# Performance work log

Measured on AMD Instinct MI355X. Metric: run time of the kernel, lower is better.

Reference implementation:

```python
import jax, jax.numpy as jnp
import numpy as np

B, N, F, H, N_ITERS = 32, 256, 8, 256, 3


def setup_inputs() -> dict:
    key = jax.random.key(0)
    ks = jax.random.split(key, 10)
    sc = lambda k, shape, fan: (jax.random.normal(k, shape, jnp.float32) / np.sqrt(fan).astype(np.float32))
    return {
        "jets": jax.random.normal(ks[0], (B, N, F), jnp.float32),
        "W_emb": sc(ks[1], (F, H), F), "b_emb": jnp.zeros((H,), jnp.float32),
        "w_edge": sc(ks[2], (H,), H), "b_edge": jnp.zeros((), jnp.float32),
        "W_msg": sc(ks[3], (H, H), H), "b_msg": jnp.zeros((H,), jnp.float32),
        "Wi": sc(ks[4], (3 * H, H + F), H + F), "bi": jnp.zeros((3 * H,), jnp.float32),
        "Wh": sc(ks[5], (3 * H, H), H), "bh": jnp.zeros((3 * H,), jnp.float32),
        "Wr1": sc(ks[6], (H, H), H), "br1": jnp.zeros((H,), jnp.float32),
        "Wr2": sc(ks[7], (H, H), H), "br2": jnp.zeros((H,), jnp.float32),
    }


def _gru(x, h, Wi, bi, Wh, bh):
    # standard torch GRUCell math; x: [B,N,H+F], h: [B,N,H]
    gi = x @ Wi.T + bi
    gh = h @ Wh.T + bh
    ir, iz, inew = jnp.split(gi, 3, axis=-1)
    hr, hz, hnew = jnp.split(gh, 3, axis=-1)
    r = jax.nn.sigmoid(ir + hr)
    z = jax.nn.sigmoid(iz + hz)
    n = jnp.tanh(inew + r * hnew)
    return (1.0 - z) * n + z * h


def reference(jets, W_emb, b_emb, w_edge, b_edge, W_msg, b_msg, Wi, bi, Wh, bh, Wr1, br1, Wr2, br2):
    h = jnp.tanh(jets @ W_emb + b_emb)  # [B,N,H]
    for _ in range(N_ITERS):
        # edge_embedding(h_l + h_r) is affine -> (h_i + h_j).w + b = s_i + s_j + b,
        # avoiding the [B,N,N,H] broadcast intermediate while computing identical scores.
        s = h @ w_edge  # [B,N]
        scores = s[:, :, None] + s[:, None, :] + b_edge  # [B,N,N]
        A = jax.nn.softmax(scores, axis=2)  # attention over sender nodes j
        msg = jnp.tanh(jnp.einsum('bij,bjh->bih', A, h @ W_msg + b_msg))
        h = _gru(jnp.concatenate([msg, jets], axis=-1), h, Wi, bi, Wh, bh)
    x = jax.nn.relu(h @ Wr1 + br1) @ Wr2 + br2  # DTNN readout per node
    return jnp.sum(x, axis=1)  # [B,H] summed over vertices
```

## Files before the change

kernel.cpp:

```cpp
#include <hip/hip_runtime.h>
#include <math.h>

#define NT 256

typedef __attribute__((ext_vector_type(8))) short short8;
typedef __attribute__((ext_vector_type(4))) float f32x4;
typedef unsigned short ushort_t;

__device__ __forceinline__ float sigmoidf_(float x){ return 1.0f/(1.0f+__expf(-x)); }
__device__ __forceinline__ ushort_t f2bf(float x){
  unsigned int u = __float_as_uint(x);
  u = u + 0x7fff + ((u>>16)&1);
  return (ushort_t)(u>>16);
}
__device__ __forceinline__ float bf2f(ushort_t b){
  return __uint_as_float(((unsigned int)b)<<16);
}

__global__ __launch_bounds__(256) void k_pe(
    const float* __restrict__ jets, const float* __restrict__ W_emb,
    const float* __restrict__ b_emb, const float* __restrict__ w_edge,
    const float* __restrict__ Wi, const float* __restrict__ bi,
    const float* __restrict__ Wh, const float* __restrict__ Wr1,
    ushort_t* __restrict__ hbf0, ushort_t* __restrict__ gjets,
    float* __restrict__ WiMt, ushort_t* __restrict__ WhB,
    ushort_t* __restrict__ Wr1T, float* __restrict__ s_part)
{
  int t = threadIdx.x, blk = blockIdx.x;
  int gid = blk*NT + t, gstride = gridDim.x*NT;
  for (int e=gid; e<256*768; e+=gstride){ int k=e/768, row=e-k*768; WiMt[e]=Wi[(size_t)row*264 + k]; }
  for (int e=gid; e<768*256; e+=gstride){ WhB[e]=f2bf(Wh[e]); }
  for (int e=gid; e<256*256; e+=gstride){ int n=e>>8, k=e&255; Wr1T[e]=f2bf(Wr1[(size_t)k*256+n]); }
  int lane = t & 63, w = t >> 6;
  #pragma unroll
  for (int v=0; v<4; ++v){
    int m = blk*16 + w*4 + v;
    float jr[8];
    #pragma unroll
    for (int f=0; f<8; ++f) jr[f] = jets[m*8+f];
    float sp = 0.f;
    #pragma unroll
    for (int u=0; u<4; ++u){
      int c = lane + 64*u;
      float a = b_emb[c];
      #pragma unroll
      for (int f=0; f<8; ++f) a = fmaf(jr[f], W_emb[f*256+c], a);
      float hv = tanhf(a);
      hbf0[(size_t)m*256 + c] = f2bf(hv);
      sp = fmaf(hv, w_edge[c], sp);
    }
    sp += __shfl_xor(sp,1); sp += __shfl_xor(sp,2); sp += __shfl_xor(sp,4);
    sp += __shfl_xor(sp,8); sp += __shfl_xor(sp,16); sp += __shfl_xor(sp,32);
    if (lane==0) s_part[m] = sp;
    else if (lane<8) s_part[lane*8192 + m] = 0.f;
    #pragma unroll
    for (int g=0; g<3; ++g){
      #pragma unroll
      for (int u=0; u<4; ++u){
        int c = lane + 64*u;
        int rowi = g*256 + c;
        float acc = bi[rowi];
        #pragma unroll
        for (int f=0; f<8; ++f) acc = fmaf(jr[f], Wi[(size_t)rowi*264 + 256 + f], acc);
        gjets[(size_t)m*768 + rowi] = f2bf(acc);
      }
    }
  }
}

__global__ __launch_bounds__(256) void k_hbar(const ushort_t* __restrict__ hbf,
    const float* __restrict__ s_part, float* __restrict__ hbar_p){
  int t = threadIdx.x;
  int b = blockIdx.x >> 3, js = blockIdx.x & 7;
  int jc = js << 5;
  __shared__ float eS[256], red[256];
  float s_t = 0.f;
  #pragma unroll
  for (int sl=0; sl<8; ++sl) s_t += s_part[sl*8192 + b*256 + t];
  red[t] = s_t; __syncthreads();
  for (int o=128;o>0;o>>=1){ if (t<o) red[t]=fmaxf(red[t],red[t+o]); __syncthreads(); }
  float mx = red[0]; __syncthreads();
  float e = __expf(s_t-mx); eS[t]=e; red[t]=e; __syncthreads();
  for (int o=128;o>0;o>>=1){ if (t<o) red[t]+=red[t+o]; __syncthreads(); }
  float rZ = 1.0f/red[0];
  const ushort_t* hb = hbf + (size_t)b*256*256;
  float p = 0.f;
  #pragma unroll
  for (int j=0;j<32;++j)
    p = fmaf(eS[jc+j], bf2f(hb[(size_t)(jc+j)*256 + t]), p);
  hbar_p[js*8192 + b*256 + t] = p*rZ;
}

__global__ __launch_bounds__(256) void k_msgp(const float* __restrict__ hbar_p,
    const float* __restrict__ W_msg, float* __restrict__ msg_p){
  int t = threadIdx.x;
  int b = blockIdx.x >> 3, ks = blockIdx.x & 7;
  __shared__ float hch[32];
  if (t < 32){
    float v = 0.f;
    #pragma unroll
    for (int sl=0; sl<8; ++sl) v += hbar_p[sl*8192 + b*256 + ks*32 + t];
    hch[t] = v;
  }
  __syncthreads();
  float acc = 0.f;
  #pragma unroll
  for (int k=0; k<32; ++k)
    acc = fmaf(hch[k], W_msg[(size_t)(ks*32+k)*256 + t], acc);
  msg_p[ks*8192 + b*256 + t] = acc;
}

__global__ __launch_bounds__(256) void k_gmsgp(const float* __restrict__ msg_p,
    const float* __restrict__ b_msg, const float* __restrict__ WiMt,
    float* __restrict__ gmsg_p){
  int t = threadIdx.x;
  int b = blockIdx.x >> 3, ks = blockIdx.x & 7;
  __shared__ float mch[32];
  if (t < 32){
    float v = b_msg[ks*32 + t];
    #pragma unroll
    for (int sl=0; sl<8; ++sl) v += msg_p[sl*8192 + b*256 + ks*32 + t];
    mch[t] = tanhf(v);
  }
  __syncthreads();
  float a0=0.f, a1=0.f, a2=0.f;
  #pragma unroll
  for (int k=0; k<32; ++k){
    float m = mch[k];
    const float* wr = &WiMt[(size_t)(ks*32+k)*768 + t];
    a0 = fmaf(m, wr[0],   a0);
    a1 = fmaf(m, wr[256], a1);
    a2 = fmaf(m, wr[512], a2);
  }
  float* gp = &gmsg_p[(size_t)ks*24576 + (size_t)b*768 + t];
  gp[0] = a0; gp[256] = a1; gp[512] = a2;
}

__global__ __launch_bounds__(256) void k_gru_mfma(
    const ushort_t* __restrict__ hbf_in,
    const ushort_t* __restrict__ WhB, const float* __restrict__ bh,
    const ushort_t* __restrict__ gjets, const float* __restrict__ gmsg_p,
    const float* __restrict__ w_edge,
    ushort_t* __restrict__ hbf_out, float* __restrict__ s_part, int compute_s)
{
  __shared__ __align__(16) short As[64*32];
  __shared__ __align__(16) short Bs[3*64*32];
  __shared__ float gm_s[192], bh_s[192];
  int t = threadIdx.x;
  int hcb = blockIdx.x & 3, mblk = blockIdx.x >> 2;
  int m0 = mblk*64, hc0 = hcb*64, b = m0 >> 8;
  if (t < 192){
    int g = t>>6, c = t&63;
    int rowi = g*256 + hc0 + c;
    float acc = 0.f;
    #pragma unroll
    for (int sl=0; sl<8; ++sl) acc += gmsg_p[(size_t)sl*24576 + (size_t)b*768 + rowi];
    gm_s[t] = acc;
    bh_s[t] = bh[rowi];
  }
  int lane = t & 63, w = t >> 6;
  int wr = w >> 1, wc = w & 1;
  int q = lane >> 4, r = lane & 15;
  int srow = t >> 2, sseg = t & 3;
  f32x4 acc[3][2][2] = {};
  for (int kt = 0; kt < 8; ++kt){
    __syncthreads();
    *(uint4*)&As[t*8] = *(const uint4*)&hbf_in[(size_t)(m0+srow)*256 + kt*32 + sseg*8];
    #pragma unroll
    for (int g = 0; g < 3; ++g)
      *(uint4*)&Bs[g*2048 + t*8] = *(const uint4*)&WhB[(size_t)(g*256 + hc0 + srow)*256 + kt*32 + sseg*8];
    __syncthreads();
    short8 af[2], bfr[3][2];
    #pragma unroll
    for (int fm=0; fm<2; ++fm)
      af[fm] = *(const short8*)&As[(wr*32 + fm*16 + r)*32 + q*8];
    #pragma unroll
    for (int g=0; g<3; ++g)
      #pragma unroll
      for (int fn=0; fn<2; ++fn)
        bfr[g][fn] = *(const short8*)&Bs[g*2048 + (wc*32 + fn*16 + r)*32 + q*8];
    #pragma unroll
    for (int g=0; g<3; ++g)
      #pragma unroll
      for (int fm=0; fm<2; ++fm)
        #pragma unroll
        for (int fn=0; fn<2; ++fn)
          acc[g][fm][fn] = __builtin_amdgcn_mfma_f32_16x16x32_bf16(af[fm], bfr[g][fn], acc[g][fm][fn], 0,0,0);
  }
  float wef[2];
  wef[0] = w_edge[hc0 + wc*32 + r];
  wef[1] = w_edge[hc0 + wc*32 + 16 + r];
  float pacc[2][4] = {};
  #pragma unroll
  for (int fm=0; fm<2; ++fm)
    #pragma unroll
    for (int fn=0; fn<2; ++fn){
      int cloc = wc*32 + fn*16 + r;
      int hcol = hc0 + cloc;
      #pragma unroll
      for (int jj=0; jj<4; ++jj){
        int m = m0 + wr*32 + fm*16 + q*4 + jj;
        float gir = bf2f(gjets[(size_t)m*768 + hcol])       + gm_s[cloc];
        float giz = bf2f(gjets[(size_t)m*768 + 256 + hcol]) + gm_s[64+cloc];
        float gin = bf2f(gjets[(size_t)m*768 + 512 + hcol]) + gm_s[128+cloc];
        float rr = sigmoidf_(gir + acc[0][fm][fn][jj] + bh_s[cloc]);
        float zz = sigmoidf_(giz + acc[1][fm][fn][jj] + bh_s[64+cloc]);
        float nn = tanhf(gin + rr*(acc[2][fm][fn][jj] + bh_s[128+cloc]));
        float ho = bf2f(hbf_in[(size_t)m*256 + hcol]);
        float hn = (1.f - zz)*nn + zz*ho;
        hbf_out[(size_t)m*256 + hcol] = f2bf(hn);
        pacc[fm][jj] = fmaf(wef[fn], hn, pacc[fm][jj]);
      }
    }
  if (compute_s){
    #pragma unroll
    for (int fm=0; fm<2; ++fm)
      #pragma unroll
      for (int jj=0; jj<4; ++jj){
        float p = pacc[fm][jj];
        p += __shfl_xor(p,1); p += __shfl_xor(p,2);
        p += __shfl_xor(p,4); p += __shfl_xor(p,8);
        if (r == 0)
          s_part[(hcb*2 + wc)*8192 + m0 + wr*32 + fm*16 + q*4 + jj] = p;
      }
  }
}

__global__ __launch_bounds__(256) void k_ro(
    const ushort_t* __restrict__ hbf, const ushort_t* __restrict__ Wr1T,
    const float* __restrict__ br1, float* __restrict__ zsum_p)
{
  __shared__ __align__(16) short As[64*32];
  __shared__ __align__(16) short Bs[64*32];
  int t = threadIdx.x;
  int ncb = blockIdx.x & 3, mblk = blockIdx.x >> 2;
  int m0 = mblk*64, nc0 = ncb*64, b = m0 >> 8;
  int lane = t & 63, w = t >> 6;
  int wr = w >> 1, wc = w & 1;
  int q = lane >> 4, r = lane & 15;
  int srow = t >> 2, sseg = t & 3;
  f32x4 acc[2][2] = {};
  for (int kt = 0; kt < 8; ++kt){
    __syncthreads();
    *(uint4*)&As[t*8] = *(const uint4*)&hbf[(size_t)(m0+srow)*256 + kt*32 + sseg*8];
    *(uint4*)&Bs[t*8] = *(const uint4*)&Wr1T[(size_t)(nc0+srow)*256 + kt*32 + sseg*8];
    __syncthreads();
    short8 af[2], bfr[2];
    #pragma unroll
    for (int fm=0; fm<2; ++fm)
      af[fm] = *(const short8*)&As[(wr*32 + fm*16 + r)*32 + q*8];
    #pragma unroll
    for (int fn=0; fn<2; ++fn)
      bfr[fn] = *(const short8*)&Bs[(wc*32 + fn*16 + r)*32 + q*8];
    #pragma unroll
    for (int fm=0; fm<2; ++fm)
      #pragma unroll
      for (int fn=0; fn<2; ++fn)
        acc[fm][fn] = __builtin_amdgcn_mfma_f32_16x16x32_bf16(af[fm], bfr[fn], acc[fm][fn], 0,0,0);
  }
  #pragma unroll
  for (int fn=0; fn<2; ++fn){
    int n = nc0 + wc*32 + fn*16 + r;
    float bb = br1[n];
    float cs = 0.f;
    #pragma unroll
    for (int fm=0; fm<2; ++fm)
      #pragma unroll
      for (int jj=0; jj<4; ++jj)
        cs += fmaxf(acc[fm][fn][jj] + bb, 0.f);
    cs += __shfl_xor(cs, 16);
    cs += __shfl_xor(cs, 32);
    if (q == 0) zsum_p[((mblk&3)*2 + wr)*8192 + b*256 + n] = cs;
  }
}

__global__ __launch_bounds__(256) void k_fin(const float* __restrict__ zsum_p,
    const float* __restrict__ Wr2, const float* __restrict__ br2,
    float* __restrict__ out){
  int b = blockIdx.x, t = threadIdx.x;
  __shared__ float zs[256];
  float z = 0.f;
  #pragma unroll
  for (int sl=0; sl<8; ++sl) z += zsum_p[sl*8192 + b*256 + t];
  zs[t] = z; __syncthreads();
  float acc = 0.f;
  for (int k=0;k<256;++k) acc = fmaf(zs[k], Wr2[k*256 + t], acc);
  out[b*256 + t] = acc + 256.0f*br2[t];
}

extern "C" void kernel_launch(void* const* d_in, const int* in_sizes, int n_in,
                              void* d_out, int out_size, void* d_ws, size_t ws_size,
                              hipStream_t stream){
  (void)in_sizes; (void)n_in; (void)out_size; (void)ws_size;
  const float* jets  = (const float*)d_in[0];
  const float* W_emb = (const float*)d_in[1];
  const float* b_emb = (const float*)d_in[2];
  const float* w_edge= (const float*)d_in[3];
  const float* W_msg = (const float*)d_in[5];
  const float* b_msg = (const float*)d_in[6];
  const float* Wi    = (const float*)d_in[7];
  const float* bi    = (const float*)d_in[8];
  const float* Wh    = (const float*)d_in[9];
  const float* bh    = (const float*)d_in[10];
  const float* Wr1   = (const float*)d_in[11];
  const float* br1   = (const float*)d_in[12];
  const float* Wr2   = (const float*)d_in[13];
  const float* br2   = (const float*)d_in[14];
  float* out = (float*)d_out;
  float* ws  = (float*)d_ws;
  ushort_t* hbf0  = (ushort_t*)ws;
  ushort_t* hbf1  = (ushort_t*)(ws + 1048576);
  ushort_t* gjets = (ushort_t*)(ws + 2097152);
  float* WiMt     = ws + 5242880;
  ushort_t* WhB   = (ushort_t*)(ws + 5439488);
  ushort_t* Wr1T  = (ushort_t*)(ws + 5537792);
  float* s_part   = ws + 5570560;
  float* hbar_p   = ws + 5636096;
  float* msg_p    = ws + 5701632;
  float* gmsg_p   = ws + 5767168;
  float* zsum_p   = ws + 5963776;
  ushort_t* hbf[2] = {hbf0, hbf1};

  k_pe<<<512,NT,0,stream>>>(jets, W_emb, b_emb, w_edge, Wi, bi, Wh, Wr1,
                            hbf[0], gjets, WiMt, WhB, Wr1T, s_part);
  for (int it=0; it<3; ++it){
    int cur = it & 1, nxt = cur ^ 1;
    k_hbar<<<256,NT,0,stream>>>(hbf[cur], s_part, hbar_p);
    k_msgp<<<256,NT,0,stream>>>(hbar_p, W_msg, msg_p);
    k_gmsgp<<<256,NT,0,stream>>>(msg_p, b_msg, WiMt, gmsg_p);
    k_gru_mfma<<<512,NT,0,stream>>>(hbf[cur], WhB, bh, gjets, gmsg_p, w_edge,
                                    hbf[nxt], s_part, (it<2)?1:0);
  }
  k_ro<<<512,NT,0,stream>>>(hbf[1], Wr1T, br1, zsum_p);
  k_fin<<<32,NT,0,stream>>>(zsum_p, Wr2, br2, out);
}
```

Baseline: 125.9 us.

## Fuse msg-to-gate projection into GRU kernel and load MFMA operands directly

Removes the separate k_gmsgp launch per iteration. Each GRU block now reduces msg partials, applies tanh, and computes its 192 gate-message values against a bf16 copy of Wi's message columns. The GRU and readout MFMA kernels drop LDS staging and barriers and read A/B fragments straight from global memory (L2-resident). This trades three launches for redundant per-block dot products (256 serial k per thread, on 192 threads) and for uncoalesced short8 global loads in place of shared tiles. It also lowers the Wi message weights to bf16 precision.

```diff
diff --git a/kernel.cpp b/kernel.cpp
--- a/kernel.cpp
+++ b/kernel.cpp
@@ -23,12 +23,12 @@
     const float* __restrict__ Wi, const float* __restrict__ bi,
     const float* __restrict__ Wh, const float* __restrict__ Wr1,
     ushort_t* __restrict__ hbf0, ushort_t* __restrict__ gjets,
-    float* __restrict__ WiMt, ushort_t* __restrict__ WhB,
+    ushort_t* __restrict__ WiMtB, ushort_t* __restrict__ WhB,
     ushort_t* __restrict__ Wr1T, float* __restrict__ s_part)
 {
   int t = threadIdx.x, blk = blockIdx.x;
   int gid = blk*NT + t, gstride = gridDim.x*NT;
-  for (int e=gid; e<256*768; e+=gstride){ int k=e/768, row=e-k*768; WiMt[e]=Wi[(size_t)row*264 + k]; }
+  for (int e=gid; e<256*768; e+=gstride){ int k=e/768, row=e-k*768; WiMtB[e]=f2bf(Wi[(size_t)row*264 + k]); }
   for (int e=gid; e<768*256; e+=gstride){ WhB[e]=f2bf(Wh[e]); }
   for (int e=gid; e<256*256; e+=gstride){ int n=e>>8, k=e&255; Wr1T[e]=f2bf(Wr1[(size_t)k*256+n]); }
   int lane = t & 63, w = t >> 6;
@@ -110,75 +110,51 @@
   msg_p[ks*8192 + b*256 + t] = acc;
 }
 
-__global__ __launch_bounds__(256) void k_gmsgp(const float* __restrict__ msg_p,
-    const float* __restrict__ b_msg, const float* __restrict__ WiMt,
-    float* __restrict__ gmsg_p){
-  int t = threadIdx.x;
-  int b = blockIdx.x >> 3, ks = blockIdx.x & 7;
-  __shared__ float mch[32];
-  if (t < 32){
-    float v = b_msg[ks*32 + t];
-    #pragma unroll
-    for (int sl=0; sl<8; ++sl) v += msg_p[sl*8192 + b*256 + ks*32 + t];
-    mch[t] = tanhf(v);
-  }
-  __syncthreads();
-  float a0=0.f, a1=0.f, a2=0.f;
-  #pragma unroll
-  for (int k=0; k<32; ++k){
-    float m = mch[k];
-    const float* wr = &WiMt[(size_t)(ks*32+k)*768 + t];
-    a0 = fmaf(m, wr[0],   a0);
-    a1 = fmaf(m, wr[256], a1);
-    a2 = fmaf(m, wr[512], a2);
-  }
-  float* gp = &gmsg_p[(size_t)ks*24576 + (size_t)b*768 + t];
-  gp[0] = a0; gp[256] = a1; gp[512] = a2;
-}
-
 __global__ __launch_bounds__(256) void k_gru_mfma(
     const ushort_t* __restrict__ hbf_in,
     const ushort_t* __restrict__ WhB, const float* __restrict__ bh,
-    const ushort_t* __restrict__ gjets, const float* __restrict__ gmsg_p,
+    const ushort_t* __restrict__ gjets, const float* __restrict__ msg_p,
+    const float* __restrict__ b_msg, const ushort_t* __restrict__ WiMtB,
     const float* __restrict__ w_edge,
     ushort_t* __restrict__ hbf_out, float* __restrict__ s_part, int compute_s)
 {
-  __shared__ __align__(16) short As[64*32];
-  __shared__ __align__(16) short Bs[3*64*32];
+  __shared__ float mvS[256];
   __shared__ float gm_s[192], bh_s[192];
   int t = threadIdx.x;
   int hcb = blockIdx.x & 3, mblk = blockIdx.x >> 2;
   int m0 = mblk*64, hc0 = hcb*64, b = m0 >> 8;
+  {
+    float v = b_msg[t];
+    #pragma unroll
+    for (int sl=0; sl<8; ++sl) v += msg_p[sl*8192 + b*256 + t];
+    mvS[t] = tanhf(v);
+  }
+  __syncthreads();
   if (t < 192){
     int g = t>>6, c = t&63;
     int rowi = g*256 + hc0 + c;
     float acc = 0.f;
-    #pragma unroll
-    for (int sl=0; sl<8; ++sl) acc += gmsg_p[(size_t)sl*24576 + (size_t)b*768 + rowi];
+    #pragma unroll 8
+    for (int k=0; k<256; ++k)
+      acc = fmaf(mvS[k], bf2f(WiMtB[(size_t)k*768 + rowi]), acc);
     gm_s[t] = acc;
     bh_s[t] = bh[rowi];
   }
   int lane = t & 63, w = t >> 6;
   int wr = w >> 1, wc = w & 1;
   int q = lane >> 4, r = lane & 15;
-  int srow = t >> 2, sseg = t & 3;
   f32x4 acc[3][2][2] = {};
+  #pragma unroll
   for (int kt = 0; kt < 8; ++kt){
-    __syncthreads();
-    *(uint4*)&As[t*8] = *(const uint4*)&hbf_in[(size_t)(m0+srow)*256 + kt*32 + sseg*8];
-    #pragma unroll
-    for (int g = 0; g < 3; ++g)
-      *(uint4*)&Bs[g*2048 + t*8] = *(const uint4*)&WhB[(size_t)(g*256 + hc0 + srow)*256 + kt*32 + sseg*8];
-    __syncthreads();
     short8 af[2], bfr[3][2];
     #pragma unroll
     for (int fm=0; fm<2; ++fm)
-      af[fm] = *(const short8*)&As[(wr*32 + fm*16 + r)*32 + q*8];
+      af[fm] = *(const short8*)&hbf_in[(size_t)(m0 + wr*32 + fm*16 + r)*256 + kt*32 + q*8];
     #pragma unroll
     for (int g=0; g<3; ++g)
       #pragma unroll
       for (int fn=0; fn<2; ++fn)
-        bfr[g][fn] = *(const short8*)&Bs[g*2048 + (wc*32 + fn*16 + r)*32 + q*8];
+        bfr[g][fn] = *(const short8*)&WhB[(size_t)(g*256 + hc0 + wc*32 + fn*16 + r)*256 + kt*32 + q*8];
     #pragma unroll
     for (int g=0; g<3; ++g)
       #pragma unroll
@@ -187,6 +163,7 @@
         for (int fn=0; fn<2; ++fn)
           acc[g][fm][fn] = __builtin_amdgcn_mfma_f32_16x16x32_bf16(af[fm], bfr[g][fn], acc[g][fm][fn], 0,0,0);
   }
+  __syncthreads();
   float wef[2];
   wef[0] = w_edge[hc0 + wc*32 + r];
   wef[1] = w_edge[hc0 + wc*32 + 16 + r];
@@ -230,28 +207,22 @@
     const ushort_t* __restrict__ hbf, const ushort_t* __restrict__ Wr1T,
     const float* __restrict__ br1, float* __restrict__ zsum_p)
 {
-  __shared__ __align__(16) short As[64*32];
-  __shared__ __align__(16) short Bs[64*32];
   int t = threadIdx.x;
   int ncb = blockIdx.x & 3, mblk = blockIdx.x >> 2;
   int m0 = mblk*64, nc0 = ncb*64, b = m0 >> 8;
   int lane = t & 63, w = t >> 6;
   int wr = w >> 1, wc = w & 1;
   int q = lane >> 4, r = lane & 15;
-  int srow = t >> 2, sseg = t & 3;
   f32x4 acc[2][2] = {};
+  #pragma unroll
   for (int kt = 0; kt < 8; ++kt){
-    __syncthreads();
-    *(uint4*)&As[t*8] = *(const uint4*)&hbf[(size_t)(m0+srow)*256 + kt*32 + sseg*8];
-    *(uint4*)&Bs[t*8] = *(const uint4*)&Wr1T[(size_t)(nc0+srow)*256 + kt*32 + sseg*8];
-    __syncthreads();
     short8 af[2], bfr[2];
     #pragma unroll
     for (int fm=0; fm<2; ++fm)
-      af[fm] = *(const short8*)&As[(wr*32 + fm*16 + r)*32 + q*8];
+      af[fm] = *(const short8*)&hbf[(size_t)(m0 + wr*32 + fm*16 + r)*256 + kt*32 + q*8];
     #pragma unroll
     for (int fn=0; fn<2; ++fn)
-      bfr[fn] = *(const short8*)&Bs[(wc*32 + fn*16 + r)*32 + q*8];
+      bfr[fn] = *(const short8*)&Wr1T[(size_t)(nc0 + wc*32 + fn*16 + r)*256 + kt*32 + q*8];
     #pragma unroll
     for (int fm=0; fm<2; ++fm)
       #pragma unroll
@@ -311,25 +282,23 @@
   ushort_t* hbf0  = (ushort_t*)ws;
   ushort_t* hbf1  = (ushort_t*)(ws + 1048576);
   ushort_t* gjets = (ushort_t*)(ws + 2097152);
-  float* WiMt     = ws + 5242880;
-  ushort_t* WhB   = (ushort_t*)(ws + 5439488);
-  ushort_t* Wr1T  = (ushort_t*)(ws + 5537792);
-  float* s_part   = ws + 5570560;
-  float* hbar_p   = ws + 5636096;
-  float* msg_p    = ws + 5701632;
-  float* gmsg_p   = ws + 5767168;
-  float* zsum_p   = ws + 5963776;
+  ushort_t* WiMtB = (ushort_t*)(ws + 5242880);
+  ushort_t* WhB   = (ushort_t*)(ws + 5341184);
+  ushort_t* Wr1T  = (ushort_t*)(ws + 5439488);
+  float* s_part   = ws + 5472256;
+  float* hbar_p   = ws + 5537792;
+  float* msg_p    = ws + 5603328;
+  float* zsum_p   = ws + 5668864;
   ushort_t* hbf[2] = {hbf0, hbf1};
 
   k_pe<<<512,NT,0,stream>>>(jets, W_emb, b_emb, w_edge, Wi, bi, Wh, Wr1,
-                            hbf[0], gjets, WiMt, WhB, Wr1T, s_part);
+                            hbf[0], gjets, WiMtB, WhB, Wr1T, s_part);
   for (int it=0; it<3; ++it){
     int cur = it & 1, nxt = cur ^ 1;
     k_hbar<<<256,NT,0,stream>>>(hbf[cur], s_part, hbar_p);
     k_msgp<<<256,NT,0,stream>>>(hbar_p, W_msg, msg_p);
-    k_gmsgp<<<256,NT,0,stream>>>(msg_p, b_msg, WiMt, gmsg_p);
-    k_gru_mfma<<<512,NT,0,stream>>>(hbf[cur], WhB, bh, gjets, gmsg_p, w_edge,
-                                    hbf[nxt], s_part, (it<2)?1:0);
+    k_gru_mfma<<<512,NT,0,stream>>>(hbf[cur], WhB, bh, gjets, msg_p, b_msg,
+                                    WiMtB, w_edge, hbf[nxt], s_part, (it<2)?1:0);
   }
   k_ro<<<512,NT,0,stream>>>(hbf[1], Wr1T, br1, zsum_p);
   k_fin<<<32,NT,0,stream>>>(zsum_p, Wr2, br2, out);
```

Measured after the change: 168.4 us. 1.34x slower.
